# Performance work log

Hardware: AMD Instinct MI355X
Metric: run time of the kernel (lower is better)

Reference implementation:

```python
import jax, jax.numpy as jnp
import numpy as np

N_NODES = 50000
N_EDGES = 800000
D_IN, D_HID, D_OUT = 128, 256, 256


def _sage_conv(x, src, dst, w_l, b_l, w_r, n_nodes):
    # PyG SAGEConv (mean aggr): out = lin_l(mean_{j in N(i)} x_j) + lin_r(x_i)
    # lin_l has bias, lin_r has no bias.
    msg_sum = jax.ops.segment_sum(x[src], dst, num_segments=n_nodes)  # [N, d]
    deg = jax.ops.segment_sum(jnp.ones_like(dst, dtype=x.dtype), dst, num_segments=n_nodes)
    agg = msg_sum / jnp.maximum(deg, 1.0)[:, None]
    return agg @ w_l.T + b_l + x @ w_r.T


def setup_inputs() -> dict:
    key = jax.random.key(0)
    ks = jax.random.split(key, 8)
    x = jax.random.normal(ks[0], (N_NODES, D_IN), dtype=jnp.float32)
    edge_index = jax.random.randint(ks[1], (2, N_EDGES), 0, N_NODES, dtype=jnp.int64)
    s1 = 1.0 / np.sqrt(D_IN)
    s2 = 1.0 / np.sqrt(D_HID)
    w_l1 = jax.random.uniform(ks[2], (D_HID, D_IN), jnp.float32, -s1, s1)
    b_l1 = jax.random.uniform(ks[3], (D_HID,), jnp.float32, -s1, s1)
    w_r1 = jax.random.uniform(ks[4], (D_HID, D_IN), jnp.float32, -s1, s1)
    w_l2 = jax.random.uniform(ks[5], (D_OUT, D_HID), jnp.float32, -s2, s2)
    b_l2 = jax.random.uniform(ks[6], (D_OUT,), jnp.float32, -s2, s2)
    w_r2 = jax.random.uniform(ks[7], (D_OUT, D_HID), jnp.float32, -s2, s2)
    return {"x": x, "edge_index": edge_index,
            "w_l1": w_l1, "b_l1": b_l1, "w_r1": w_r1,
            "w_l2": w_l2, "b_l2": b_l2, "w_r2": w_r2}


def reference(x, edge_index, w_l1, b_l1, w_r1, w_l2, b_l2, w_r2):
    src, dst = edge_index[0], edge_index[1]
    h = jax.nn.relu(_sage_conv(x, src, dst, w_l1, b_l1, w_r1, N_NODES))
    out = jax.nn.relu(_sage_conv(h, src, dst, w_l2, b_l2, w_r2, N_NODES))
    return out
```

## Files before the change

### kernel.cpp

```cpp
#include <hip/hip_runtime.h>
#include <stdint.h>

#define N_NODES 50000
#define N_EDGES 800000
#define BCAP 128

typedef __attribute__((ext_vector_type(8))) short bf16x8;
typedef __attribute__((ext_vector_type(4))) float f32x4;

__device__ __forceinline__ float bf2f(unsigned short u) {
    return __builtin_bit_cast(float, (unsigned int)u << 16);
}
__device__ __forceinline__ unsigned short f2bf(float f) {
    unsigned int u = __builtin_bit_cast(unsigned int, f);
    u += 0x7fffu + ((u >> 16) & 1u);
    return (unsigned short)(u >> 16);
}

__device__ __forceinline__ void load_lds16(const void* g, void* l) {
    __builtin_amdgcn_global_load_lds(
        (const __attribute__((address_space(1))) void*)(uintptr_t)g,
        (__attribute__((address_space(3))) void*)(unsigned int)(uintptr_t)l,
        16, 0, 0);
}

__global__ __launch_bounds__(256) void build_buckets_k(
    const int* __restrict__ src, const int* __restrict__ dst,
    int* __restrict__ cnt, int* __restrict__ bucket, int nedges)
{
    int e = blockIdx.x * 256 + threadIdx.x;
    if (e >= nedges) return;
    int d = dst[e];
    int p = atomicAdd(&cnt[d], 1);
    if (p < BCAP) bucket[(size_t)d * BCAP + p] = src[e];
}

__global__ __launch_bounds__(256) void invdeg_k(
    const int* __restrict__ cnt, float* __restrict__ invdeg, int n)
{
    int i = blockIdx.x * 256 + threadIdx.x;
    if (i < n) {
        int d = cnt[i];
        invdeg[i] = 1.0f / (float)(d > 1 ? d : 1);
    }
}

__global__ __launch_bounds__(256) void cvt_x_k(
    const float* __restrict__ x, unsigned short* __restrict__ dst)
{
    int tid = blockIdx.x * 256 + threadIdx.x;
    if (tid >= N_NODES * 32) return;
    int row = tid >> 5, c = (tid & 31) * 4;
    float4 v = *(const float4*)(x + (size_t)row * 128 + c);
    ushort4 o;
    o.x = f2bf(v.x); o.y = f2bf(v.y); o.z = f2bf(v.z); o.w = f2bf(v.w);
    *(ushort4*)(dst + (size_t)row * 256 + 128 + c) = o;
}

__global__ __launch_bounds__(256) void cvt_w_k(
    const float* __restrict__ wl, const float* __restrict__ wr,
    unsigned short* __restrict__ dst, int Keach)
{
    int tid = blockIdx.x * 256 + threadIdx.x;
    if (tid >= 256 * 2 * Keach) return;
    int n = tid / (2 * Keach), k = tid - n * 2 * Keach;
    float v = (k < Keach) ? wl[(size_t)n * Keach + k]
                          : wr[(size_t)n * Keach + (k - Keach)];
    dst[tid] = f2bf(v);
}

__device__ __forceinline__ void acc8(float* a, uint4 u) {
    a[0] += bf2f((unsigned short)u.x); a[1] += bf2f((unsigned short)(u.x >> 16));
    a[2] += bf2f((unsigned short)u.y); a[3] += bf2f((unsigned short)(u.y >> 16));
    a[4] += bf2f((unsigned short)u.z); a[5] += bf2f((unsigned short)(u.z >> 16));
    a[6] += bf2f((unsigned short)u.w); a[7] += bf2f((unsigned short)(u.w >> 16));
}

template <int CPR>
__global__ __launch_bounds__(256) void agg_k(
    const unsigned short* __restrict__ feat, int featStride,
    const int* __restrict__ bucket, const int* __restrict__ cnt,
    const float* __restrict__ invdeg,
    unsigned short* __restrict__ outmsg, int outStride, int nnodes)
{
    constexpr int E = 64 / CPR;
    int wv = threadIdx.x >> 6, lane = threadIdx.x & 63;
    int node = blockIdx.x * 4 + wv;
    if (node >= nnodes) return;
    int deg = cnt[node]; if (deg > BCAP) deg = BCAP;
    int idx0 = bucket[(size_t)node * BCAP + lane];
    int idx1 = bucket[(size_t)node * BCAP + 64 + lane];
    const int sub = lane / CPR;
    const int col = lane & (CPR - 1);

    float acc[8] = {};
    auto getsrc = [&](int e) -> int {
        return (e < 64) ? __shfl(idx0, e) : __shfl(idx1, e - 64);
    };
    auto rowp = [&](int s) -> const uint4* {
        return (const uint4*)(feat + (size_t)s * featStride + col * 8);
    };

    int j = 0;
    for (; j + 4 * E <= deg; j += 4 * E) {
        int s0 = getsrc(j + sub), s1 = getsrc(j + E + sub);
        int s2 = getsrc(j + 2 * E + sub), s3 = getsrc(j + 3 * E + sub);
        uint4 u0 = *rowp(s0), u1 = *rowp(s1), u2 = *rowp(s2), u3 = *rowp(s3);
        acc8(acc, u0); acc8(acc, u1); acc8(acc, u2); acc8(acc, u3);
    }
    for (; j + 2 * E <= deg; j += 2 * E) {
        int s0 = getsrc(j + sub), s1 = getsrc(j + E + sub);
        uint4 u0 = *rowp(s0), u1 = *rowp(s1);
        acc8(acc, u0); acc8(acc, u1);
    }
    for (; j + E <= deg; j += E) {
        uint4 u0 = *rowp(getsrc(j + sub));
        acc8(acc, u0);
    }
    if (j < deg) {
        int e = j + sub;
        int ec = (e < deg) ? e : (deg - 1);
        uint4 u0 = *rowp(getsrc(ec));
        if (e < deg) acc8(acc, u0);
    }

#pragma unroll
    for (int stride = 32; stride >= CPR; stride >>= 1) {
#pragma unroll
        for (int v = 0; v < 8; v++) acc[v] += __shfl_xor(acc[v], stride);
    }

    if (lane < CPR) {
        float s = invdeg[node];
        uint4 o;
        o.x = (unsigned int)f2bf(acc[0] * s) | ((unsigned int)f2bf(acc[1] * s) << 16);
        o.y = (unsigned int)f2bf(acc[2] * s) | ((unsigned int)f2bf(acc[3] * s) << 16);
        o.z = (unsigned int)f2bf(acc[4] * s) | ((unsigned int)f2bf(acc[5] * s) << 16);
        o.w = (unsigned int)f2bf(acc[6] * s) | ((unsigned int)f2bf(acc[7] * s) << 16);
        *(uint4*)(outmsg + (size_t)node * outStride + lane * 8) = o;
    }
}

template <bool BF16OUT>
__global__ __launch_bounds__(256) void gemm_k(
    const unsigned short* __restrict__ A, const unsigned short* __restrict__ W,
    const float* __restrict__ bias, void* __restrict__ outp, int outStride,
    int M, int K)
{
    __shared__ __align__(16) char smem[(128 + 128) * 64];
    const int t = threadIdx.x;
    const int w = t >> 6, lane = t & 63;
    const int quad = lane >> 4, l15 = lane & 15;
    const int row0 = blockIdx.x * 128;
    const int col0 = blockIdx.y * 128;

    f32x4 acc[2][8] = {};

    for (int ks = 0; ks < K; ks += 32) {
#pragma unroll
        for (int j = 0; j < 4; j++) {
            int call = w * 4 + j;
            int ci = call * 64 + lane;
            const unsigned short* g;
            if (call < 8) {
                int rg = row0 + (ci >> 2);
                if (rg > M - 1) rg = M - 1;
                g = A + (size_t)rg * K + ks + (ci & 3) * 8;
            } else {
                int c2 = ci - 512;
                g = W + (size_t)(col0 + (c2 >> 2)) * K + ks + (c2 & 3) * 8;
            }
            load_lds16(g, smem + ci * 16);
        }
        __syncthreads();

        const char* Ab = smem + (w * 32 + l15) * 64 + quad * 16;
        const char* Wb = smem + 8192 + l15 * 64 + quad * 16;
        bf16x8 af0 = *(const bf16x8*)(Ab);
        bf16x8 af1 = *(const bf16x8*)(Ab + 1024);
#pragma unroll
        for (int tt = 0; tt < 8; tt++) {
            bf16x8 bfr = *(const bf16x8*)(Wb + tt * 1024);
            acc[0][tt] = __builtin_amdgcn_mfma_f32_16x16x32_bf16(af0, bfr, acc[0][tt], 0, 0, 0);
            acc[1][tt] = __builtin_amdgcn_mfma_f32_16x16x32_bf16(af1, bfr, acc[1][tt], 0, 0, 0);
        }
        __syncthreads();
    }

#pragma unroll
    for (int g = 0; g < 2; g++) {
#pragma unroll
        for (int tt = 0; tt < 8; tt++) {
            int col = col0 + tt * 16 + l15;
            float bv = bias[col];
#pragma unroll
            for (int i = 0; i < 4; i++) {
                int row = row0 + w * 32 + g * 16 + quad * 4 + i;
                if (row < M) {
                    float v = fmaxf(acc[g][tt][i] + bv, 0.f);
                    size_t off = (size_t)row * outStride + col;
                    if constexpr (BF16OUT) ((unsigned short*)outp)[off] = f2bf(v);
                    else                   ((float*)outp)[off] = v;
                }
            }
        }
    }
}

extern "C" void kernel_launch(void* const* d_in, const int* in_sizes, int n_in,
                              void* d_out, int out_size, void* d_ws, size_t ws_size,
                              hipStream_t stream)
{
    const float* x   = (const float*)d_in[0];
    const int*   ei  = (const int*)d_in[1];
    const float* wl1 = (const float*)d_in[2];
    const float* bl1 = (const float*)d_in[3];
    const float* wr1 = (const float*)d_in[4];
    const float* wl2 = (const float*)d_in[5];
    const float* bl2 = (const float*)d_in[6];
    const float* wr2 = (const float*)d_in[7];
    float* out = (float*)d_out;
    const int* src = ei;
    const int* dst = ei + N_EDGES;

    char* ws = (char*)d_ws;
    size_t off = 0;
    auto alloc = [&](size_t bytes) -> void* {
        void* p = ws + off;
        off = (off + bytes + 255) & ~(size_t)255;
        return p;
    };
    int*            cnt    = (int*)           alloc((size_t)N_NODES * 4);
    int*            bucket = (int*)           alloc((size_t)N_NODES * BCAP * 4);
    float*          invdeg = (float*)         alloc((size_t)N_NODES * 4);
    unsigned short* Acat1  = (unsigned short*)alloc((size_t)N_NODES * 256 * 2);
    unsigned short* Acat2  = (unsigned short*)alloc((size_t)N_NODES * 512 * 2);
    unsigned short* Wcat1  = (unsigned short*)alloc((size_t)256 * 256 * 2);
    unsigned short* Wcat2  = (unsigned short*)alloc((size_t)256 * 512 * 2);

    hipMemsetAsync(cnt, 0, (size_t)N_NODES * 4, stream);
    build_buckets_k<<<(N_EDGES + 255) / 256, 256, 0, stream>>>(src, dst, cnt, bucket, N_EDGES);
    invdeg_k<<<(N_NODES + 255) / 256, 256, 0, stream>>>(cnt, invdeg, N_NODES);

    cvt_x_k<<<(N_NODES * 32 + 255) / 256, 256, 0, stream>>>(x, Acat1);
    cvt_w_k<<<(256 * 256 + 255) / 256, 256, 0, stream>>>(wl1, wr1, Wcat1, 128);
    cvt_w_k<<<(256 * 512 + 255) / 256, 256, 0, stream>>>(wl2, wr2, Wcat2, 256);

    agg_k<16><<<(N_NODES + 3) / 4, 256, 0, stream>>>(
        Acat1 + 128, 256, bucket, cnt, invdeg, Acat1, 256, N_NODES);
    gemm_k<true><<<dim3((N_NODES + 127) / 128, 2), 256, 0, stream>>>(
        Acat1, Wcat1, bl1, (void*)(Acat2 + 256), 512, N_NODES, 256);

    agg_k<32><<<(N_NODES + 3) / 4, 256, 0, stream>>>(
        Acat2 + 256, 512, bucket, cnt, invdeg, Acat2, 512, N_NODES);
    gemm_k<false><<<dim3((N_NODES + 127) / 128, 2), 256, 0, stream>>>(
        Acat2, Wcat2, bl2, (void*)out, 256, N_NODES, 512);
}
```

Measured before the change: 307.7 us.

## Sort each node's neighbor bucket by source-index segment for gather locality

```diff
diff --git a/kernel.cpp b/kernel.cpp
--- a/kernel.cpp
+++ b/kernel.cpp
@@ -4,6 +4,8 @@
 #define N_NODES 50000
 #define N_EDGES 800000
 #define BCAP 128
+#define NSEG 8
+#define SEGSZ 6250
 
 typedef __attribute__((ext_vector_type(8))) short bf16x8;
 typedef __attribute__((ext_vector_type(4))) float f32x4;
@@ -24,25 +26,43 @@
         16, 0, 0);
 }
 
-__global__ __launch_bounds__(256) void build_buckets_k(
+__global__ __launch_bounds__(256) void count_k(
     const int* __restrict__ src, const int* __restrict__ dst,
-    int* __restrict__ cnt, int* __restrict__ bucket, int nedges)
+    int* __restrict__ cnt8, int nedges)
 {
     int e = blockIdx.x * 256 + threadIdx.x;
     if (e >= nedges) return;
-    int d = dst[e];
-    int p = atomicAdd(&cnt[d], 1);
-    if (p < BCAP) bucket[(size_t)d * BCAP + p] = src[e];
-}
-
-__global__ __launch_bounds__(256) void invdeg_k(
-    const int* __restrict__ cnt, float* __restrict__ invdeg, int n)
+    int d = dst[e], s = src[e];
+    int seg = s / SEGSZ;
+    atomicAdd(&cnt8[seg * N_NODES + d], 1);
+}
+
+__global__ __launch_bounds__(256) void offs_k(
+    const int* __restrict__ cnt8, int* __restrict__ cur8,
+    int* __restrict__ degtot, float* __restrict__ invdeg, int n)
 {
     int i = blockIdx.x * 256 + threadIdx.x;
-    if (i < n) {
-        int d = cnt[i];
-        invdeg[i] = 1.0f / (float)(d > 1 ? d : 1);
-    }
+    if (i >= n) return;
+    int run = 0;
+#pragma unroll
+    for (int s = 0; s < NSEG; s++) {
+        cur8[s * N_NODES + i] = i * BCAP + run;
+        run += cnt8[s * N_NODES + i];
+    }
+    degtot[i] = run;
+    invdeg[i] = 1.0f / (float)(run > 1 ? run : 1);
+}
+
+__global__ __launch_bounds__(256) void scatter_k(
+    const int* __restrict__ src, const int* __restrict__ dst,
+    int* __restrict__ cur8, int* __restrict__ bucket, int nedges)
+{
+    int e = blockIdx.x * 256 + threadIdx.x;
+    if (e >= nedges) return;
+    int d = dst[e], s = src[e];
+    int seg = s / SEGSZ;
+    int p = atomicAdd(&cur8[seg * N_NODES + d], 1);
+    if (p < d * BCAP + BCAP) bucket[p] = s;
 }
 
 __global__ __launch_bounds__(256) void cvt_x_k(
@@ -79,7 +99,7 @@
 template <int CPR>
 __global__ __launch_bounds__(256) void agg_k(
     const unsigned short* __restrict__ feat, int featStride,
-    const int* __restrict__ bucket, const int* __restrict__ cnt,
+    const int* __restrict__ bucket, const int* __restrict__ degtot,
     const float* __restrict__ invdeg,
     unsigned short* __restrict__ outmsg, int outStride, int nnodes)
 {
@@ -87,7 +107,7 @@
     int wv = threadIdx.x >> 6, lane = threadIdx.x & 63;
     int node = blockIdx.x * 4 + wv;
     if (node >= nnodes) return;
-    int deg = cnt[node]; if (deg > BCAP) deg = BCAP;
+    int deg = degtot[node]; if (deg > BCAP) deg = BCAP;
     int idx0 = bucket[(size_t)node * BCAP + lane];
     int idx1 = bucket[(size_t)node * BCAP + 64 + lane];
     const int sub = lane / CPR;
@@ -230,7 +250,9 @@
         off = (off + bytes + 255) & ~(size_t)255;
         return p;
     };
-    int*            cnt    = (int*)           alloc((size_t)N_NODES * 4);
+    int*            cnt8   = (int*)           alloc((size_t)NSEG * N_NODES * 4);
+    int*            cur8   = (int*)           alloc((size_t)NSEG * N_NODES * 4);
+    int*            degtot = (int*)           alloc((size_t)N_NODES * 4);
     int*            bucket = (int*)           alloc((size_t)N_NODES * BCAP * 4);
     float*          invdeg = (float*)         alloc((size_t)N_NODES * 4);
     unsigned short* Acat1  = (unsigned short*)alloc((size_t)N_NODES * 256 * 2);
@@ -238,21 +260,22 @@
     unsigned short* Wcat1  = (unsigned short*)alloc((size_t)256 * 256 * 2);
     unsigned short* Wcat2  = (unsigned short*)alloc((size_t)256 * 512 * 2);
 
-    hipMemsetAsync(cnt, 0, (size_t)N_NODES * 4, stream);
-    build_buckets_k<<<(N_EDGES + 255) / 256, 256, 0, stream>>>(src, dst, cnt, bucket, N_EDGES);
-    invdeg_k<<<(N_NODES + 255) / 256, 256, 0, stream>>>(cnt, invdeg, N_NODES);
+    hipMemsetAsync(cnt8, 0, (size_t)NSEG * N_NODES * 4, stream);
+    count_k<<<(N_EDGES + 255) / 256, 256, 0, stream>>>(src, dst, cnt8, N_EDGES);
+    offs_k<<<(N_NODES + 255) / 256, 256, 0, stream>>>(cnt8, cur8, degtot, invdeg, N_NODES);
+    scatter_k<<<(N_EDGES + 255) / 256, 256, 0, stream>>>(src, dst, cur8, bucket, N_EDGES);
 
     cvt_x_k<<<(N_NODES * 32 + 255) / 256, 256, 0, stream>>>(x, Acat1);
     cvt_w_k<<<(256 * 256 + 255) / 256, 256, 0, stream>>>(wl1, wr1, Wcat1, 128);
     cvt_w_k<<<(256 * 512 + 255) / 256, 256, 0, stream>>>(wl2, wr2, Wcat2, 256);
 
     agg_k<16><<<(N_NODES + 3) / 4, 256, 0, stream>>>(
-        Acat1 + 128, 256, bucket, cnt, invdeg, Acat1, 256, N_NODES);
+        Acat1 + 128, 256, bucket, degtot, invdeg, Acat1, 256, N_NODES);
     gemm_k<true><<<dim3((N_NODES + 127) / 128, 2), 256, 0, stream>>>(
         Acat1, Wcat1, bl1, (void*)(Acat2 + 256), 512, N_NODES, 256);
 
     agg_k<32><<<(N_NODES + 3) / 4, 256, 0, stream>>>(
-        Acat2 + 256, 512, bucket, cnt, invdeg, Acat2, 512, N_NODES);
+        Acat2 + 256, 512, bucket, degtot, invdeg, Acat2, 512, N_NODES);
     gemm_k<false><<<dim3((N_NODES + 127) / 128, 2), 256, 0, stream>>>(
         Acat2, Wcat2, bl2, (void*)out, 256, N_NODES, 512);
 }
```

Measured after the change: 348.6 us. 13.3% more time.

## Partition edge bucketing, cut bucket cap, gather layer-2 features as fp8

Applied to the files above, without the earlier changes.

```diff
diff --git a/kernel.cpp b/kernel.cpp
--- a/kernel.cpp
+++ b/kernel.cpp
@@ -3,7 +3,9 @@
 
 #define N_NODES 50000
 #define N_EDGES 800000
-#define BCAP 128
+#define BCAP 64
+#define NPART 391
+#define PCAP 2560
 
 typedef __attribute__((ext_vector_type(8))) short bf16x8;
 typedef __attribute__((ext_vector_type(4))) float f32x4;
@@ -15,6 +17,24 @@
     unsigned int u = __builtin_bit_cast(unsigned int, f);
     u += 0x7fffu + ((u >> 16) & 1u);
     return (unsigned short)(u >> 16);
+}
+
+__device__ __forceinline__ unsigned char f2fp8(float f) {
+    f = fminf(f, 448.f);
+    if (f < 0.015625f) {
+        return (unsigned char)(int)__builtin_rintf(f * 512.f);
+    }
+    unsigned int u = __builtin_bit_cast(unsigned int, f);
+    u += 0x7FFFFu + ((u >> 20) & 1u);
+    return (unsigned char)((u >> 20) - 960u);
+}
+__device__ __forceinline__ void accf8x4(float* a, unsigned int w) {
+#pragma unroll
+    for (int b = 0; b < 4; b++) {
+        unsigned int c = (w >> (8 * b)) & 0xFFu;
+        float n = __builtin_bit_cast(float, 0x3C000000u + (c << 20));
+        a[b] += (c < 8u) ? (float)c * 0.001953125f : n;
+    }
 }
 
 __device__ __forceinline__ void load_lds16(const void* g, void* l) {
@@ -24,24 +44,43 @@
         16, 0, 0);
 }
 
-__global__ __launch_bounds__(256) void build_buckets_k(
+__global__ __launch_bounds__(256) void part_append_k(
     const int* __restrict__ src, const int* __restrict__ dst,
-    int* __restrict__ cnt, int* __restrict__ bucket, int nedges)
+    int* __restrict__ pcnt, uint2* __restrict__ pbuf, int nedges)
 {
     int e = blockIdx.x * 256 + threadIdx.x;
     if (e >= nedges) return;
-    int d = dst[e];
-    int p = atomicAdd(&cnt[d], 1);
-    if (p < BCAP) bucket[(size_t)d * BCAP + p] = src[e];
-}
-
-__global__ __launch_bounds__(256) void invdeg_k(
-    const int* __restrict__ cnt, float* __restrict__ invdeg, int n)
-{
-    int i = blockIdx.x * 256 + threadIdx.x;
-    if (i < n) {
-        int d = cnt[i];
-        invdeg[i] = 1.0f / (float)(d > 1 ? d : 1);
+    int s = src[e], d = dst[e];
+    int part = d >> 7;
+    int pos = atomicAdd(&pcnt[part], 1);
+    if (pos < PCAP) pbuf[(size_t)part * PCAP + pos] = make_uint2((unsigned)s, (unsigned)d);
+}
+
+__global__ __launch_bounds__(256) void part_bucket_k(
+    const int* __restrict__ pcnt, const uint2* __restrict__ pbuf,
+    int* __restrict__ bucket, int* __restrict__ degtot, float* __restrict__ invdeg)
+{
+    __shared__ int lcnt[128];
+    int part = blockIdx.x, tid = threadIdx.x;
+    if (tid < 128) lcnt[tid] = 0;
+    __syncthreads();
+    int n = pcnt[part];
+    if (n > PCAP) n = PCAP;
+    const uint2* pb = pbuf + (size_t)part * PCAP;
+    for (int i = tid; i < n; i += 256) {
+        uint2 pr = pb[i];
+        int d = (int)pr.y;
+        int p = atomicAdd(&lcnt[d & 127], 1);
+        if (p < BCAP) bucket[(size_t)d * BCAP + p] = (int)pr.x;
+    }
+    __syncthreads();
+    if (tid < 128) {
+        int node = part * 128 + tid;
+        if (node < N_NODES) {
+            int c = lcnt[tid];
+            degtot[node] = (c > BCAP) ? BCAP : c;
+            invdeg[node] = 1.0f / (float)(c > 1 ? c : 1);
+        }
     }
 }
 
@@ -76,76 +115,126 @@
     a[6] += bf2f((unsigned short)u.w); a[7] += bf2f((unsigned short)(u.w >> 16));
 }
 
-template <int CPR>
-__global__ __launch_bounds__(256) void agg_k(
-    const unsigned short* __restrict__ feat, int featStride,
-    const int* __restrict__ bucket, const int* __restrict__ cnt,
+__global__ __launch_bounds__(256) void agg1_k(
+    const unsigned short* __restrict__ feat,
+    const int* __restrict__ bucket, const int* __restrict__ degtot,
     const float* __restrict__ invdeg,
-    unsigned short* __restrict__ outmsg, int outStride, int nnodes)
-{
-    constexpr int E = 64 / CPR;
+    unsigned short* __restrict__ outmsg)
+{
     int wv = threadIdx.x >> 6, lane = threadIdx.x & 63;
     int node = blockIdx.x * 4 + wv;
-    if (node >= nnodes) return;
-    int deg = cnt[node]; if (deg > BCAP) deg = BCAP;
+    if (node >= N_NODES) return;
+    int deg = degtot[node];
     int idx0 = bucket[(size_t)node * BCAP + lane];
-    int idx1 = bucket[(size_t)node * BCAP + 64 + lane];
-    const int sub = lane / CPR;
-    const int col = lane & (CPR - 1);
+    const int sub = lane >> 4;
+    const int col = lane & 15;
 
     float acc[8] = {};
-    auto getsrc = [&](int e) -> int {
-        return (e < 64) ? __shfl(idx0, e) : __shfl(idx1, e - 64);
-    };
-    auto rowp = [&](int s) -> const uint4* {
-        return (const uint4*)(feat + (size_t)s * featStride + col * 8);
-    };
+    auto rowp = [&](int s) { return (const uint4*)(feat + (size_t)s * 256 + col * 8); };
 
     int j = 0;
-    for (; j + 4 * E <= deg; j += 4 * E) {
-        int s0 = getsrc(j + sub), s1 = getsrc(j + E + sub);
-        int s2 = getsrc(j + 2 * E + sub), s3 = getsrc(j + 3 * E + sub);
+    for (; j + 16 <= deg; j += 16) {
+        int s0 = __shfl(idx0, j + sub),     s1 = __shfl(idx0, j + 4 + sub);
+        int s2 = __shfl(idx0, j + 8 + sub), s3 = __shfl(idx0, j + 12 + sub);
         uint4 u0 = *rowp(s0), u1 = *rowp(s1), u2 = *rowp(s2), u3 = *rowp(s3);
         acc8(acc, u0); acc8(acc, u1); acc8(acc, u2); acc8(acc, u3);
     }
-    for (; j + 2 * E <= deg; j += 2 * E) {
-        int s0 = getsrc(j + sub), s1 = getsrc(j + E + sub);
+    for (; j + 8 <= deg; j += 8) {
+        int s0 = __shfl(idx0, j + sub), s1 = __shfl(idx0, j + 4 + sub);
         uint4 u0 = *rowp(s0), u1 = *rowp(s1);
         acc8(acc, u0); acc8(acc, u1);
     }
-    for (; j + E <= deg; j += E) {
-        uint4 u0 = *rowp(getsrc(j + sub));
+    for (; j + 4 <= deg; j += 4) {
+        uint4 u0 = *rowp(__shfl(idx0, j + sub));
         acc8(acc, u0);
     }
     if (j < deg) {
         int e = j + sub;
         int ec = (e < deg) ? e : (deg - 1);
-        uint4 u0 = *rowp(getsrc(ec));
+        uint4 u0 = *rowp(__shfl(idx0, ec));
         if (e < deg) acc8(acc, u0);
     }
-
-#pragma unroll
-    for (int stride = 32; stride >= CPR; stride >>= 1) {
+#pragma unroll
+    for (int stride = 32; stride >= 16; stride >>= 1)
 #pragma unroll
         for (int v = 0; v < 8; v++) acc[v] += __shfl_xor(acc[v], stride);
-    }
-
-    if (lane < CPR) {
+
+    if (lane < 16) {
         float s = invdeg[node];
         uint4 o;
         o.x = (unsigned int)f2bf(acc[0] * s) | ((unsigned int)f2bf(acc[1] * s) << 16);
         o.y = (unsigned int)f2bf(acc[2] * s) | ((unsigned int)f2bf(acc[3] * s) << 16);
         o.z = (unsigned int)f2bf(acc[4] * s) | ((unsigned int)f2bf(acc[5] * s) << 16);
         o.w = (unsigned int)f2bf(acc[6] * s) | ((unsigned int)f2bf(acc[7] * s) << 16);
-        *(uint4*)(outmsg + (size_t)node * outStride + lane * 8) = o;
-    }
-}
-
-template <bool BF16OUT>
+        *(uint4*)(outmsg + (size_t)node * 256 + lane * 8) = o;
+    }
+}
+
+__device__ __forceinline__ void acc16f8(float* a, uint4 u) {
+    accf8x4(a + 0, u.x); accf8x4(a + 4, u.y); accf8x4(a + 8, u.z); accf8x4(a + 12, u.w);
+}
+
+__global__ __launch_bounds__(256) void agg2_k(
+    const unsigned char* __restrict__ hf8,
+    const int* __restrict__ bucket, const int* __restrict__ degtot,
+    const float* __restrict__ invdeg,
+    unsigned short* __restrict__ outmsg)
+{
+    int wv = threadIdx.x >> 6, lane = threadIdx.x & 63;
+    int node = blockIdx.x * 4 + wv;
+    if (node >= N_NODES) return;
+    int deg = degtot[node];
+    int idx0 = bucket[(size_t)node * BCAP + lane];
+    const int sub = lane >> 4;
+    const int col = lane & 15;
+
+    float acc[16] = {};
+    auto rowp = [&](int s) { return (const uint4*)(hf8 + (size_t)s * 256 + col * 16); };
+
+    int j = 0;
+    for (; j + 16 <= deg; j += 16) {
+        int s0 = __shfl(idx0, j + sub),     s1 = __shfl(idx0, j + 4 + sub);
+        int s2 = __shfl(idx0, j + 8 + sub), s3 = __shfl(idx0, j + 12 + sub);
+        uint4 u0 = *rowp(s0), u1 = *rowp(s1), u2 = *rowp(s2), u3 = *rowp(s3);
+        acc16f8(acc, u0); acc16f8(acc, u1); acc16f8(acc, u2); acc16f8(acc, u3);
+    }
+    for (; j + 8 <= deg; j += 8) {
+        int s0 = __shfl(idx0, j + sub), s1 = __shfl(idx0, j + 4 + sub);
+        uint4 u0 = *rowp(s0), u1 = *rowp(s1);
+        acc16f8(acc, u0); acc16f8(acc, u1);
+    }
+    for (; j + 4 <= deg; j += 4) {
+        uint4 u0 = *rowp(__shfl(idx0, j + sub));
+        acc16f8(acc, u0);
+    }
+    if (j < deg) {
+        int e = j + sub;
+        int ec = (e < deg) ? e : (deg - 1);
+        uint4 u0 = *rowp(__shfl(idx0, ec));
+        if (e < deg) acc16f8(acc, u0);
+    }
+#pragma unroll
+    for (int stride = 32; stride >= 16; stride >>= 1)
+#pragma unroll
+        for (int v = 0; v < 16; v++) acc[v] += __shfl_xor(acc[v], stride);
+
+    if (lane < 16) {
+        float s = invdeg[node];
+        unsigned int o[8];
+#pragma unroll
+        for (int v = 0; v < 8; v++)
+            o[v] = (unsigned int)f2bf(acc[2 * v] * s) | ((unsigned int)f2bf(acc[2 * v + 1] * s) << 16);
+        unsigned short* wp = outmsg + (size_t)node * 512 + lane * 16;
+        *(uint4*)(wp)     = make_uint4(o[0], o[1], o[2], o[3]);
+        *(uint4*)(wp + 8) = make_uint4(o[4], o[5], o[6], o[7]);
+    }
+}
+
+template <bool BF16OUT, bool WRITE_FP8>
 __global__ __launch_bounds__(256) void gemm_k(
     const unsigned short* __restrict__ A, const unsigned short* __restrict__ W,
     const float* __restrict__ bias, void* __restrict__ outp, int outStride,
-    int M, int K)
+    unsigned char* __restrict__ hf8, int M, int K)
 {
     __shared__ __align__(16) char smem[(128 + 128) * 64];
     const int t = threadIdx.x;
@@ -201,6 +290,7 @@
                     size_t off = (size_t)row * outStride + col;
                     if constexpr (BF16OUT) ((unsigned short*)outp)[off] = f2bf(v);
                     else                   ((float*)outp)[off] = v;
+                    if constexpr (WRITE_FP8) hf8[(size_t)row * 256 + col] = f2fp8(v);
                 }
             }
         }
@@ -230,29 +320,32 @@
         off = (off + bytes + 255) & ~(size_t)255;
         return p;
     };
-    int*            cnt    = (int*)           alloc((size_t)N_NODES * 4);
+    int*            pcnt   = (int*)           alloc((size_t)NPART * 4);
+    uint2*          pbuf   = (uint2*)         alloc((size_t)NPART * PCAP * 8);
     int*            bucket = (int*)           alloc((size_t)N_NODES * BCAP * 4);
+    int*            degtot = (int*)           alloc((size_t)N_NODES * 4);
     float*          invdeg = (float*)         alloc((size_t)N_NODES * 4);
     unsigned short* Acat1  = (unsigned short*)alloc((size_t)N_NODES * 256 * 2);
     unsigned short* Acat2  = (unsigned short*)alloc((size_t)N_NODES * 512 * 2);
+    unsigned char*  hf8    = (unsigned char*) alloc((size_t)N_NODES * 256);
     unsigned short* Wcat1  = (unsigned short*)alloc((size_t)256 * 256 * 2);
     unsigned short* Wcat2  = (unsigned short*)alloc((size_t)256 * 512 * 2);
 
-    hipMemsetAsync(cnt, 0, (size_t)N_NODES * 4, stream);
-    build_buckets_k<<<(N_EDGES + 255) / 256, 256, 0, stream>>>(src, dst, cnt, bucket, N_EDGES);
-    invdeg_k<<<(N_NODES + 255) / 256, 256, 0, stream>>>(cnt, invdeg, N_NODES);
+    hipMemsetAsync(pcnt, 0, (size_t)NPART * 4, stream);
+    part_append_k<<<(N_EDGES + 255) / 256, 256, 0, stream>>>(src, dst, pcnt, pbuf, N_EDGES);
+    part_bucket_k<<<NPART, 256, 0, stream>>>(pcnt, pbuf, bucket, degtot, invdeg);
 
     cvt_x_k<<<(N_NODES * 32 + 255) / 256, 256, 0, stream>>>(x, Acat1);
     cvt_w_k<<<(256 * 256 + 255) / 256, 256, 0, stream>>>(wl1, wr1, Wcat1, 128);
     cvt_w_k<<<(256 * 512 + 255) / 256, 256, 0, stream>>>(wl2, wr2, Wcat2, 256);
 
-    agg_k<16><<<(N_NODES + 3) / 4, 256, 0, stream>>>(
-        Acat1 + 128, 256, bucket, cnt, invdeg, Acat1, 256, N_NODES);
-    gemm_k<true><<<dim3((N_NODES + 127) / 128, 2), 256, 0, stream>>>(
-        Acat1, Wcat1, bl1, (void*)(Acat2 + 256), 512, N_NODES, 256);
-
-    agg_k<32><<<(N_NODES + 3) / 4, 256, 0, stream>>>(
-        Acat2 + 256, 512, bucket, cnt, invdeg, Acat2, 512, N_NODES);
-    gemm_k<false><<<dim3((N_NODES + 127) / 128, 2), 256, 0, stream>>>(
-        Acat2, Wcat2, bl2, (void*)out, 256, N_NODES, 512);
-}
+    agg1_k<<<(N_NODES + 3) / 4, 256, 0, stream>>>(
+        Acat1 + 128, bucket, degtot, invdeg, Acat1);
+    gemm_k<true, true><<<dim3((N_NODES + 127) / 128, 2), 256, 0, stream>>>(
+        Acat1, Wcat1, bl1, (void*)(Acat2 + 256), 512, hf8, N_NODES, 256);
+
+    agg2_k<<<(N_NODES + 3) / 4, 256, 0, stream>>>(
+        hf8, bucket, degtot, invdeg, Acat2);
+    gemm_k<false, false><<<dim3((N_NODES + 127) / 128, 2), 256, 0, stream>>>(
+        Acat2, Wcat2, bl2, (void*)out, 256, nullptr, N_NODES, 512);
+}
```

After: 562.6 us. 82.9% more time.
